# Performance work log

Measured on AMD Instinct MI355X. Metric: run time of the kernel, lower is better.

Reference implementation:

```python
import jax, jax.numpy as jnp
import numpy as np

N_NODES = 100000
N_EDGES = 3200000
N_GRAPHS = 64
NEG_SLOPE = 0.2


def mish(x):
    return x * jnp.tanh(jax.nn.softplus(x))


def gat_layer(x, src, dst, W, b, a_src, a_dst, heads, out_ch, n_nodes):
    # h: [N, H, C]
    h = (x @ W).reshape(n_nodes, heads, out_ch)
    alpha_s = jnp.sum(h * a_src[None], axis=-1)  # [N, H]
    alpha_d = jnp.sum(h * a_dst[None], axis=-1)  # [N, H]
    e = jax.nn.leaky_relu(alpha_s[src] + alpha_d[dst], NEG_SLOPE)  # [E, H]
    # scatter-softmax over incoming edges of each destination node
    emax = jax.ops.segment_max(e, dst, num_segments=n_nodes)  # [N, H]
    ee = jnp.exp(e - emax[dst])
    den = jax.ops.segment_sum(ee, dst, num_segments=n_nodes)
    alpha = ee / (den[dst] + 1e-16)  # [E, H]
    msg = h[src] * alpha[..., None]  # [E, H, C]
    out = jax.ops.segment_sum(msg, dst, num_segments=n_nodes)
    return out.reshape(n_nodes, heads * out_ch) + b


def setup_inputs() -> dict:
    key = jax.random.key(0)
    ks = jax.random.split(key, 10)
    x = jax.random.normal(ks[0], (N_NODES, 128), dtype=jnp.float32)
    edge_index = jax.random.randint(ks[1], (2, N_EDGES), 0, N_NODES, dtype=jnp.int64)
    batch = jnp.sort(jax.random.randint(ks[2], (N_NODES,), 0, N_GRAPHS, dtype=jnp.int64))
    s1 = 1.0 / np.sqrt(128.0)
    s2 = 1.0 / np.sqrt(16.0)
    return {
        "x": x,
        "edge_index": edge_index,
        "batch": batch,
        "W1": jax.random.normal(ks[3], (128, 16), dtype=jnp.float32) * s1,
        "b1": jnp.zeros((16,), dtype=jnp.float32),
        "a_src1": jax.random.normal(ks[4], (4, 4), dtype=jnp.float32) * 0.5,
        "a_dst1": jax.random.normal(ks[5], (4, 4), dtype=jnp.float32) * 0.5,
        "W2": jax.random.normal(ks[6], (16, 32), dtype=jnp.float32) * s2,
        "b2": jnp.zeros((32,), dtype=jnp.float32),
        "a_src2": jax.random.normal(ks[7], (1, 32), dtype=jnp.float32) * 0.5,
        "a_dst2": jax.random.normal(ks[8], (1, 32), dtype=jnp.float32) * 0.5,
    }


def reference(x, edge_index, batch, W1, b1, a_src1, a_dst1, W2, b2, a_src2, a_dst2):
    n = x.shape[0]
    # PyG GATConv default add_self_loops=True
    loop = jnp.arange(n, dtype=edge_index.dtype)
    src = jnp.concatenate([edge_index[0], loop])
    dst = jnp.concatenate([edge_index[1], loop])
    h = mish(gat_layer(x, src, dst, W1, b1, a_src1, a_dst1, heads=4, out_ch=4, n_nodes=n))
    h = mish(gat_layer(h, src, dst, W2, b2, a_src2, a_dst2, heads=1, out_ch=32, n_nodes=n))
    # global_mean_pool
    sums = jax.ops.segment_sum(h, batch, num_segments=N_GRAPHS)
    cnts = jax.ops.segment_sum(jnp.ones((n,), h.dtype), batch, num_segments=N_GRAPHS)
    return sums / jnp.maximum(cnts, 1.0)[:, None]
```

## Files before the change

kernel.cpp:

```cpp
#include <hip/hip_runtime.h>
#include <hip/hip_fp16.h>
#include <math.h>

#define NEG_SLOPE 0.2f
#define SB 256
#define NBMAX 1024

typedef _Float16 half2v __attribute__((ext_vector_type(2)));

__device__ __forceinline__ float mishf(float x) {
    if (x > 15.f) return x;
    float ex = __expf(x);
    float y = 1.f + ex;
    float y2 = y * y;
    return x * (y2 - 1.f) / (y2 + 1.f);
}

__device__ __forceinline__ float lw(float e) {
    return __expf(fmaxf(e, NEG_SLOPE * e));
}

__device__ __forceinline__ float hdot2(half2v a, half2v b) {
#if __has_builtin(__builtin_amdgcn_fdot2)
    return __builtin_amdgcn_fdot2(a, b, 0.f, false);
#else
    return (float)a.x * (float)b.x + (float)a.y * (float)b.y;
#endif
}

__global__ void gemm1_kernel(const float* __restrict__ x, const float* __restrict__ W1,
                             const float* __restrict__ a_dst,
                             _Float16* __restrict__ hpre1h, float* __restrict__ addst,
                             int* __restrict__ bucket_total, float* __restrict__ pool,
                             float* __restrict__ cnt, int NB, int NG, int N) {
    __shared__ float Wl[128 * 16];
    __shared__ float xs[16 * 132];
    int tid = threadIdx.x;
    if (blockIdx.x == 0) {
        for (int i = tid; i < NB; i += 256) bucket_total[i] = 0;
        for (int i = tid; i < NG * 32; i += 256) pool[i] = 0.f;
        for (int i = tid; i < NG; i += 256) cnt[i] = 0.f;
    }
    for (int i = tid; i < 2048; i += 256) Wl[i] = W1[i];
    int nodebase = blockIdx.x * 16;
    const float4* x4 = (const float4*)(x + (size_t)nodebase * 128);
    for (int i = tid; i < 512; i += 256) {
        float4 v = x4[i];
        int e = i * 4;
        int nl = e >> 7, k = e & 127;
        float* dp = &xs[nl * 132 + k];
        dp[0] = v.x; dp[1] = v.y; dp[2] = v.z; dp[3] = v.w;
    }
    __syncthreads();
    int nl = tid >> 4, ch = tid & 15;
    const float* xr = &xs[nl * 132];
    float acc = 0.f;
    #pragma unroll 8
    for (int k = 0; k < 128; k++) acc += xr[k] * Wl[k * 16 + ch];
    int node = nodebase + nl;
    if (node < N) {
        hpre1h[node * 16 + ch] = (_Float16)acc;
        float pd = acc * a_dst[ch];
        pd += __shfl_xor(pd, 1); pd += __shfl_xor(pd, 2);
        if ((ch & 3) == 0) addst[node * 4 + (ch >> 2)] = pd;
    }
}

__global__ __launch_bounds__(1024) void histB_kernel(
        const int* __restrict__ dst, int E, int Etot, int CH, int NB,
        int* __restrict__ hist, int* __restrict__ bucket_total) {
    __shared__ int cnt[NBMAX];
    int tid = threadIdx.x, blk = blockIdx.x;
    for (int b = tid; b < NB; b += 1024) cnt[b] = 0;
    __syncthreads();
    int iend = min((blk + 1) * CH, Etot);
    for (int i = blk * CH + tid; i < iend; i += 1024) {
        int d = (i < E) ? dst[i] : (i - E);
        atomicAdd(&cnt[d >> 7], 1);
    }
    __syncthreads();
    for (int b = tid; b < NB; b += 1024) {
        int c = cnt[b];
        hist[b * SB + blk] = c;
        if (c) atomicAdd(&bucket_total[b], c);
    }
}

__global__ __launch_bounds__(1024) void setup_kernel(
        const int* __restrict__ bucket_total, int NB,
        int* __restrict__ bucket_base, int* __restrict__ cursor,
        const float* __restrict__ W2, const float* __restrict__ as2,
        const float* __restrict__ ad2, float* __restrict__ vs, float* __restrict__ vd) {
    __shared__ int s[1024];
    int t = threadIdx.x;
    int own = (t < NB) ? bucket_total[t] : 0;
    s[t] = own;
    __syncthreads();
    for (int off = 1; off < 1024; off <<= 1) {
        int v = (t >= off) ? s[t - off] : 0;
        __syncthreads();
        s[t] += v;
        __syncthreads();
    }
    if (t < NB) {
        int ex = s[t] - own;
        bucket_base[t] = ex;
        cursor[t] = ex;
    }
    if (t < 16) {
        float ps = 0.f, pd = 0.f;
        #pragma unroll
        for (int c = 0; c < 32; c++) {
            float w = W2[t * 32 + c];
            ps += w * as2[c];
            pd += w * ad2[c];
        }
        vs[t] = ps; vd[t] = pd;
    }
}

__global__ __launch_bounds__(1024) void scatE2_kernel(
        const int* __restrict__ src, const int* __restrict__ dst,
        int E, int Etot, int CH, int NB,
        const int* __restrict__ hist, int* __restrict__ cursor,
        int* __restrict__ pairs) {
    __shared__ int lcnt[NBMAX];
    __shared__ int lbase[NBMAX];
    int tid = threadIdx.x, blk = blockIdx.x;
    for (int b = tid; b < NB; b += 1024) {
        lcnt[b] = 0;
        int h = hist[b * SB + blk];
        lbase[b] = h ? atomicAdd(&cursor[b], h) : 0;
    }
    __syncthreads();
    int iend = min((blk + 1) * CH, Etot);
    for (int i = blk * CH + tid; i < iend; i += 1024) {
        int s, d;
        if (i < E) { s = src[i]; d = dst[i]; } else { s = d = i - E; }
        int b = d >> 7, dl = d & 127;
        int r = atomicAdd(&lcnt[b], 1);
        pairs[lbase[b] + r] = s | (dl << 17);
    }
}

__global__ __launch_bounds__(1024) void localcsr_kernel(
        const int* __restrict__ pairs, const int* __restrict__ bucket_base,
        const int* __restrict__ bucket_total, int NB, int N,
        int* __restrict__ ssorted, int* __restrict__ row_start) {
    __shared__ int deg[128];
    __shared__ int s[128];
    __shared__ int cur[128];
    int tid = threadIdx.x, b = blockIdx.x;
    int nb0 = b << 7;
    int cnt_nodes = min(128, N - nb0);
    int start = bucket_base[b];
    int end = start + bucket_total[b];
    if (tid < 128) deg[tid] = 0;
    __syncthreads();
    for (int j = start + tid; j < end; j += 1024)
        atomicAdd(&deg[(pairs[j] >> 17) & 127], 1);
    __syncthreads();
    if (tid < 128) s[tid] = deg[tid];
    __syncthreads();
    for (int o = 1; o < 128; o <<= 1) {
        int v = 0;
        if (tid < 128 && tid >= o) v = s[tid - o];
        __syncthreads();
        if (tid < 128) s[tid] += v;
        __syncthreads();
    }
    if (tid < 128) {
        int ex = start + s[tid] - deg[tid];
        cur[tid] = ex;
        if (tid < cnt_nodes) row_start[nb0 + tid] = ex;
    }
    if (b == NB - 1 && tid == 0) row_start[N] = end;
    __syncthreads();
    for (int j = start + tid; j < end; j += 1024) {
        int p = pairs[j];
        int pos = atomicAdd(&cur[(p >> 17) & 127], 1);
        ssorted[pos] = p & 0x1FFFF;
    }
}

__global__ void agg1_kernel(const int* __restrict__ row_start, const int* __restrict__ ssorted,
                            const float* __restrict__ a_src1, const float* __restrict__ addst,
                            const _Float16* __restrict__ hpre1h,
                            const float* __restrict__ b1,
                            const float* __restrict__ vs, const float* __restrict__ vd,
                            _Float16* __restrict__ hpost1h,
                            float* __restrict__ as2n, float* __restrict__ ad2n, int N) {
    int wave = threadIdx.x >> 6;
    int lane = threadIdx.x & 63;
    int node = blockIdx.x * 4 + wave;
    if (node >= N) return;
    int start = row_start[node], end = row_start[node + 1];
    int er = lane >> 3, hc = lane & 7, head = hc >> 1;
    int c0 = hc * 2;
    half2v wsh;
    wsh.x = (_Float16)a_src1[c0];
    wsh.y = (_Float16)a_src1[c0 + 1];
    float adh = addst[node * 4 + head];
    const _Float16* hb = hpre1h + c0;
    float den = 0.f, a0 = 0.f, a1 = 0.f;
    int last = end - 1;
    int jb = start;
    for (; jb + 16 <= end; jb += 16) {
        int j0 = jb + er, j1 = j0 + 8;
        int s0 = __builtin_nontemporal_load(ssorted + j0);
        int s1 = __builtin_nontemporal_load(ssorted + j1);
        half2v h0 = *(const half2v*)(hb + s0 * 16);
        half2v h1 = *(const half2v*)(hb + s1 * 16);
        float p0 = hdot2(h0, wsh);
        float p1 = hdot2(h1, wsh);
        float w0 = lw(p0 + __shfl_xor(p0, 1) + adh);
        float w1 = lw(p1 + __shfl_xor(p1, 1) + adh);
        den += w0 + w1;
        a0 += (float)h0.x * w0 + (float)h1.x * w1;
        a1 += (float)h0.y * w0 + (float)h1.y * w1;
    }
    if (jb < end) {
        int j0 = jb + er, j1 = j0 + 8;
        int k0 = (j0 <= last) ? j0 : last;
        int k1 = (j1 <= last) ? j1 : last;
        int s0 = __builtin_nontemporal_load(ssorted + k0);
        int s1 = __builtin_nontemporal_load(ssorted + k1);
        half2v h0 = *(const half2v*)(hb + s0 * 16);
        half2v h1 = *(const half2v*)(hb + s1 * 16);
        float p0 = hdot2(h0, wsh);
        float p1 = hdot2(h1, wsh);
        float e0 = p0 + __shfl_xor(p0, 1) + adh;
        float e1 = p1 + __shfl_xor(p1, 1) + adh;
        float w0 = (j0 <= last) ? lw(e0) : 0.f;
        float w1 = (j1 <= last) ? lw(e1) : 0.f;
        den += w0 + w1;
        a0 += (float)h0.x * w0 + (float)h1.x * w1;
        a1 += (float)h0.y * w0 + (float)h1.y * w1;
    }
    a0 += __shfl_xor(a0, 8);  a1 += __shfl_xor(a1, 8);  den += __shfl_xor(den, 8);
    a0 += __shfl_xor(a0, 16); a1 += __shfl_xor(a1, 16); den += __shfl_xor(den, 16);
    a0 += __shfl_xor(a0, 32); a1 += __shfl_xor(a1, 32); den += __shfl_xor(den, 32);
    if (er == 0) {
        float inv = 1.f / (den + 1e-16f);
        float o0 = mishf(a0 * inv + b1[c0]);
        float o1 = mishf(a1 * inv + b1[c0 + 1]);
        half2v oh;
        oh.x = (_Float16)o0; oh.y = (_Float16)o1;
        *(half2v*)(hpost1h + node * 16 + c0) = oh;
        float ps = o0 * vs[c0] + o1 * vs[c0 + 1];
        float pd = o0 * vd[c0] + o1 * vd[c0 + 1];
        ps += __shfl_xor(ps, 1); pd += __shfl_xor(pd, 1);
        ps += __shfl_xor(ps, 2); pd += __shfl_xor(pd, 2);
        ps += __shfl_xor(ps, 4); pd += __shfl_xor(pd, 4);
        if (hc == 0) { as2n[node] = ps; ad2n[node] = pd; }
    }
}

__global__ void agg2_kernel(const int* __restrict__ row_start, const int* __restrict__ ssorted,
                            const float* __restrict__ as2n, const float* __restrict__ ad2n,
                            const _Float16* __restrict__ hpost1h,
                            float* __restrict__ agg16, float* __restrict__ denv, int N) {
    int wave = threadIdx.x >> 6;
    int lane = threadIdx.x & 63;
    int node = blockIdx.x * 4 + wave;
    if (node >= N) return;
    int start = row_start[node], end = row_start[node + 1];
    int er = lane >> 3, hc = lane & 7;
    int c0 = hc * 2;
    float adh = ad2n[node];
    const _Float16* hb = hpost1h + c0;
    float den = 0.f, a0 = 0.f, a1 = 0.f;
    int last = end - 1;
    int jb = start;
    for (; jb + 16 <= end; jb += 16) {
        int j0 = jb + er, j1 = j0 + 8;
        int s0 = __builtin_nontemporal_load(ssorted + j0);
        int s1 = __builtin_nontemporal_load(ssorted + j1);
        float e0 = as2n[s0] + adh;
        float e1 = as2n[s1] + adh;
        half2v h0 = *(const half2v*)(hb + s0 * 16);
        half2v h1 = *(const half2v*)(hb + s1 * 16);
        float w0 = lw(e0);
        float w1 = lw(e1);
        den += w0 + w1;
        a0 += (float)h0.x * w0 + (float)h1.x * w1;
        a1 += (float)h0.y * w0 + (float)h1.y * w1;
    }
    if (jb < end) {
        int j0 = jb + er, j1 = j0 + 8;
        int k0 = (j0 <= last) ? j0 : last;
        int k1 = (j1 <= last) ? j1 : last;
        int s0 = __builtin_nontemporal_load(ssorted + k0);
        int s1 = __builtin_nontemporal_load(ssorted + k1);
        float e0 = as2n[s0] + adh;
        float e1 = as2n[s1] + adh;
        half2v h0 = *(const half2v*)(hb + s0 * 16);
        half2v h1 = *(const half2v*)(hb + s1 * 16);
        float w0 = (j0 <= last) ? lw(e0) : 0.f;
        float w1 = (j1 <= last) ? lw(e1) : 0.f;
        den += w0 + w1;
        a0 += (float)h0.x * w0 + (float)h1.x * w1;
        a1 += (float)h0.y * w0 + (float)h1.y * w1;
    }
    a0 += __shfl_xor(a0, 8);  a1 += __shfl_xor(a1, 8);  den += __shfl_xor(den, 8);
    a0 += __shfl_xor(a0, 16); a1 += __shfl_xor(a1, 16); den += __shfl_xor(den, 16);
    a0 += __shfl_xor(a0, 32); a1 += __shfl_xor(a1, 32); den += __shfl_xor(den, 32);
    if (er == 0) {
        float2 o; o.x = a0; o.y = a1;
        *(float2*)(agg16 + node * 16 + c0) = o;
        if (hc == 0) denv[node] = den;
    }
}

__global__ void post2_kernel(const float* __restrict__ agg16, const float* __restrict__ denv,
                             const float* __restrict__ W2, const float* __restrict__ b2,
                             float* __restrict__ hpost2, int N) {
    __shared__ float Wl[16 * 32];
    __shared__ float hs[8 * 20];
    __shared__ float dsh[8];
    int tid = threadIdx.x;
    for (int i = tid; i < 512; i += 256) Wl[i] = W2[i];
    int nodebase = blockIdx.x * 8;
    const float4* h4 = (const float4*)(agg16 + (size_t)nodebase * 16);
    if (tid < 32) {
        float4 v = h4[tid];
        int e = tid * 4;
        int nl = e >> 4, k = e & 15;
        float* dp = &hs[nl * 20 + k];
        dp[0] = v.x; dp[1] = v.y; dp[2] = v.z; dp[3] = v.w;
    }
    if (tid < 8) {
        int n = nodebase + tid;
        dsh[tid] = denv[(n < N) ? n : (N - 1)];
    }
    __syncthreads();
    int nl = tid >> 5, ch = tid & 31;
    const float* hr = &hs[nl * 20];
    float acc = 0.f;
    #pragma unroll
    for (int k = 0; k < 16; k++) acc += hr[k] * Wl[k * 32 + ch];
    int node = nodebase + nl;
    if (node < N) {
        float val = acc / (dsh[nl] + 1e-16f) + b2[ch];
        hpost2[(size_t)node * 32 + ch] = mishf(val);
    }
}

__global__ void pool_kernel(const float* __restrict__ hpost2, const int* __restrict__ batch,
                            int N, float* __restrict__ pool, float* __restrict__ cnt) {
    int tid = threadIdx.x;
    int r = tid >> 5, ch = tid & 31;
    int base = blockIdx.x * 512;
    int cur = -1;
    float sum = 0.f, c = 0.f;
    for (int it = 0; it < 64; it++) {
        int n = base + it * 8 + r;
        if (n >= N) break;
        int g = batch[n];
        if (g != cur) {
            if (cur >= 0) {
                atomicAdd(&pool[cur * 32 + ch], sum);
                if (ch == 0) atomicAdd(&cnt[cur], c);
            }
            cur = g; sum = 0.f; c = 0.f;
        }
        sum += hpost2[(size_t)n * 32 + ch];
        c += 1.f;
    }
    if (cur >= 0) {
        atomicAdd(&pool[cur * 32 + ch], sum);
        if (ch == 0) atomicAdd(&cnt[cur], c);
    }
}

__global__ void fin_kernel(const float* __restrict__ pool, const float* __restrict__ cnt,
                           float* __restrict__ out, int NG) {
    int i = blockIdx.x * blockDim.x + threadIdx.x;
    if (i >= NG * 32) return;
    out[i] = pool[i] / fmaxf(cnt[i >> 5], 1.0f);
}

extern "C" void kernel_launch(void* const* d_in, const int* in_sizes, int n_in,
                              void* d_out, int out_size, void* d_ws, size_t ws_size,
                              hipStream_t stream) {
    const float* x   = (const float*)d_in[0];
    const int* eidx  = (const int*)d_in[1];
    const int* batch = (const int*)d_in[2];
    const float* W1  = (const float*)d_in[3];
    const float* b1  = (const float*)d_in[4];
    const float* as1 = (const float*)d_in[5];
    const float* ad1 = (const float*)d_in[6];
    const float* W2  = (const float*)d_in[7];
    const float* b2  = (const float*)d_in[8];
    const float* as2 = (const float*)d_in[9];
    const float* ad2 = (const float*)d_in[10];
    float* out = (float*)d_out;

    int N = in_sizes[0] / 128;
    int E = in_sizes[1] / 2;
    int Etot = E + N;
    int NG = out_size / 32;
    const int* esrc = eidx;
    const int* edst = eidx + E;

    int NB = (N + 127) >> 7;
    int CH = (Etot + SB - 1) / SB;
    int T  = NB * SB;

    char* p = (char*)d_ws;
    auto alloc = [&](size_t nbytes) {
        p = (char*)(((uintptr_t)p + 15) & ~(uintptr_t)15);
        void* r = (void*)p; p += nbytes; return r;
    };
    int* hist         = (int*)alloc((size_t)T * 4);
    int* pairs        = (int*)alloc((size_t)Etot * 4);
    int* ssorted      = (int*)alloc((size_t)Etot * 4);
    int* row_start    = (int*)alloc((size_t)(N + 1) * 4);
    int* bucket_total = (int*)alloc((size_t)NB * 4);
    int* bucket_base  = (int*)alloc((size_t)NB * 4);
    int* cursor       = (int*)alloc((size_t)NB * 4);
    _Float16* hpre1h  = (_Float16*)alloc((size_t)N * 16 * 2);
    _Float16* hpost1h = (_Float16*)alloc((size_t)N * 16 * 2);
    float* addst1  = (float*)alloc((size_t)N * 4 * 4);
    float* as2n    = (float*)alloc((size_t)N * 4);
    float* ad2n    = (float*)alloc((size_t)N * 4);
    float* agg16   = (float*)alloc((size_t)N * 16 * 4);
    float* denv    = (float*)alloc((size_t)N * 4);
    float* hpost2  = (float*)alloc((size_t)N * 32 * 4);
    float* vs      = (float*)alloc(16 * 4);
    float* vd      = (float*)alloc(16 * 4);
    float* pool    = (float*)alloc((size_t)NG * 32 * 4);
    float* cnt     = (float*)alloc((size_t)NG * 4);

    gemm1_kernel<<<(N + 15) / 16, 256, 0, stream>>>(x, W1, ad1, hpre1h, addst1,
                                                    bucket_total, pool, cnt, NB, NG, N);
    histB_kernel<<<SB, 1024, 0, stream>>>(edst, E, Etot, CH, NB, hist, bucket_total);
    setup_kernel<<<1, 1024, 0, stream>>>(bucket_total, NB, bucket_base, cursor,
                                         W2, as2, ad2, vs, vd);
    scatE2_kernel<<<SB, 1024, 0, stream>>>(esrc, edst, E, Etot, CH, NB, hist, cursor, pairs);
    localcsr_kernel<<<NB, 1024, 0, stream>>>(pairs, bucket_base, bucket_total, NB, N,
                                             ssorted, row_start);
    agg1_kernel<<<(N + 3) / 4, 256, 0, stream>>>(row_start, ssorted, as1, addst1, hpre1h,
                                                 b1, vs, vd, hpost1h, as2n, ad2n, N);
    agg2_kernel<<<(N + 3) / 4, 256, 0, stream>>>(row_start, ssorted, as2n, ad2n, hpost1h,
                                                 agg16, denv, N);
    post2_kernel<<<(N + 7) / 8, 256, 0, stream>>>(agg16, denv, W2, b2, hpost2, N);
    pool_kernel<<<(N + 511) / 512, 256, 0, stream>>>(hpost2, batch, N, pool, cnt);
    fin_kernel<<<(NG * 32 + 255) / 256, 256, 0, stream>>>(pool, cnt, out, NG);
}
```

Before: 377.5 us.

## Fuse CSR build with layer-1 aggregation and post2 with pooling

The local CSR construction kernel now goes straight on to aggregate layer 1 for its 128-node bucket. Each of its 16 waves handles 8 nodes, reading the edge slice just written to ssorted, which is likely still in cache. The post-GEMM/mish of layer 2 is folded into the pooling kernel, so the N×32 hpost2 buffer is no longer written and re-read. Fewer launches and less memory traffic are traded for less parallelism in agg1 (782 blocks of 1024 threads) and serialized node processing per wave.

Measured after the change: 372.0 us. Within noise of the previous version (-1.4%).

```diff
diff --git a/kernel.cpp b/kernel.cpp
--- a/kernel.cpp
+++ b/kernel.cpp
@@ -143,21 +143,26 @@
     }
 }
 
-__global__ __launch_bounds__(1024) void localcsr_kernel(
+__global__ __launch_bounds__(1024) void csragg1_kernel(
         const int* __restrict__ pairs, const int* __restrict__ bucket_base,
         const int* __restrict__ bucket_total, int NB, int N,
-        int* __restrict__ ssorted, int* __restrict__ row_start) {
+        int* __restrict__ ssorted, int* __restrict__ row_start,
+        const float* __restrict__ a_src1, const float* __restrict__ addst,
+        const _Float16* __restrict__ hpre1h, const float* __restrict__ b1,
+        const float* __restrict__ vs, const float* __restrict__ vd,
+        _Float16* __restrict__ hpost1h,
+        float* __restrict__ as2n, float* __restrict__ ad2n) {
     __shared__ int deg[128];
     __shared__ int s[128];
     __shared__ int cur[128];
     int tid = threadIdx.x, b = blockIdx.x;
     int nb0 = b << 7;
     int cnt_nodes = min(128, N - nb0);
-    int start = bucket_base[b];
-    int end = start + bucket_total[b];
+    int bstart = bucket_base[b];
+    int bend = bstart + bucket_total[b];
     if (tid < 128) deg[tid] = 0;
     __syncthreads();
-    for (int j = start + tid; j < end; j += 1024)
+    for (int j = bstart + tid; j < bend; j += 1024)
         atomicAdd(&deg[(pairs[j] >> 17) & 127], 1);
     __syncthreads();
     if (tid < 128) s[tid] = deg[tid];
@@ -170,89 +175,86 @@
         __syncthreads();
     }
     if (tid < 128) {
-        int ex = start + s[tid] - deg[tid];
+        int ex = bstart + s[tid] - deg[tid];
         cur[tid] = ex;
         if (tid < cnt_nodes) row_start[nb0 + tid] = ex;
     }
-    if (b == NB - 1 && tid == 0) row_start[N] = end;
-    __syncthreads();
-    for (int j = start + tid; j < end; j += 1024) {
+    if (b == NB - 1 && tid == 0) row_start[N] = bend;
+    __syncthreads();
+    for (int j = bstart + tid; j < bend; j += 1024) {
         int p = pairs[j];
         int pos = atomicAdd(&cur[(p >> 17) & 127], 1);
         ssorted[pos] = p & 0x1FFFF;
     }
-}
-
-__global__ void agg1_kernel(const int* __restrict__ row_start, const int* __restrict__ ssorted,
-                            const float* __restrict__ a_src1, const float* __restrict__ addst,
-                            const _Float16* __restrict__ hpre1h,
-                            const float* __restrict__ b1,
-                            const float* __restrict__ vs, const float* __restrict__ vd,
-                            _Float16* __restrict__ hpost1h,
-                            float* __restrict__ as2n, float* __restrict__ ad2n, int N) {
-    int wave = threadIdx.x >> 6;
-    int lane = threadIdx.x & 63;
-    int node = blockIdx.x * 4 + wave;
-    if (node >= N) return;
-    int start = row_start[node], end = row_start[node + 1];
+    __syncthreads();
+
+    int wave = tid >> 6;
+    int lane = tid & 63;
     int er = lane >> 3, hc = lane & 7, head = hc >> 1;
     int c0 = hc * 2;
     half2v wsh;
     wsh.x = (_Float16)a_src1[c0];
     wsh.y = (_Float16)a_src1[c0 + 1];
-    float adh = addst[node * 4 + head];
     const _Float16* hb = hpre1h + c0;
-    float den = 0.f, a0 = 0.f, a1 = 0.f;
-    int last = end - 1;
-    int jb = start;
-    for (; jb + 16 <= end; jb += 16) {
-        int j0 = jb + er, j1 = j0 + 8;
-        int s0 = __builtin_nontemporal_load(ssorted + j0);
-        int s1 = __builtin_nontemporal_load(ssorted + j1);
-        half2v h0 = *(const half2v*)(hb + s0 * 16);
-        half2v h1 = *(const half2v*)(hb + s1 * 16);
-        float p0 = hdot2(h0, wsh);
-        float p1 = hdot2(h1, wsh);
-        float w0 = lw(p0 + __shfl_xor(p0, 1) + adh);
-        float w1 = lw(p1 + __shfl_xor(p1, 1) + adh);
-        den += w0 + w1;
-        a0 += (float)h0.x * w0 + (float)h1.x * w1;
-        a1 += (float)h0.y * w0 + (float)h1.y * w1;
-    }
-    if (jb < end) {
-        int j0 = jb + er, j1 = j0 + 8;
-        int k0 = (j0 <= last) ? j0 : last;
-        int k1 = (j1 <= last) ? j1 : last;
-        int s0 = __builtin_nontemporal_load(ssorted + k0);
-        int s1 = __builtin_nontemporal_load(ssorted + k1);
-        half2v h0 = *(const half2v*)(hb + s0 * 16);
-        half2v h1 = *(const half2v*)(hb + s1 * 16);
-        float p0 = hdot2(h0, wsh);
-        float p1 = hdot2(h1, wsh);
-        float e0 = p0 + __shfl_xor(p0, 1) + adh;
-        float e1 = p1 + __shfl_xor(p1, 1) + adh;
-        float w0 = (j0 <= last) ? lw(e0) : 0.f;
-        float w1 = (j1 <= last) ? lw(e1) : 0.f;
-        den += w0 + w1;
-        a0 += (float)h0.x * w0 + (float)h1.x * w1;
-        a1 += (float)h0.y * w0 + (float)h1.y * w1;
-    }
-    a0 += __shfl_xor(a0, 8);  a1 += __shfl_xor(a1, 8);  den += __shfl_xor(den, 8);
-    a0 += __shfl_xor(a0, 16); a1 += __shfl_xor(a1, 16); den += __shfl_xor(den, 16);
-    a0 += __shfl_xor(a0, 32); a1 += __shfl_xor(a1, 32); den += __shfl_xor(den, 32);
-    if (er == 0) {
-        float inv = 1.f / (den + 1e-16f);
-        float o0 = mishf(a0 * inv + b1[c0]);
-        float o1 = mishf(a1 * inv + b1[c0 + 1]);
-        half2v oh;
-        oh.x = (_Float16)o0; oh.y = (_Float16)o1;
-        *(half2v*)(hpost1h + node * 16 + c0) = oh;
-        float ps = o0 * vs[c0] + o1 * vs[c0 + 1];
-        float pd = o0 * vd[c0] + o1 * vd[c0 + 1];
-        ps += __shfl_xor(ps, 1); pd += __shfl_xor(pd, 1);
-        ps += __shfl_xor(ps, 2); pd += __shfl_xor(pd, 2);
-        ps += __shfl_xor(ps, 4); pd += __shfl_xor(pd, 4);
-        if (hc == 0) { as2n[node] = ps; ad2n[node] = pd; }
+    for (int r = 0; r < 8; r++) {
+        int ln = (wave << 3) + r;
+        if (ln >= cnt_nodes) break;
+        int node = nb0 + ln;
+        int end = cur[ln];
+        int start = end - deg[ln];
+        float adh = addst[node * 4 + head];
+        float den = 0.f, a0 = 0.f, a1 = 0.f;
+        int last = end - 1;
+        int jb = start;
+        for (; jb + 16 <= end; jb += 16) {
+            int j0 = jb + er, j1 = j0 + 8;
+            int s0 = ssorted[j0];
+            int s1 = ssorted[j1];
+            half2v h0 = *(const half2v*)(hb + s0 * 16);
+            half2v h1 = *(const half2v*)(hb + s1 * 16);
+            float p0 = hdot2(h0, wsh);
+            float p1 = hdot2(h1, wsh);
+            float w0 = lw(p0 + __shfl_xor(p0, 1) + adh);
+            float w1 = lw(p1 + __shfl_xor(p1, 1) + adh);
+            den += w0 + w1;
+            a0 += (float)h0.x * w0 + (float)h1.x * w1;
+            a1 += (float)h0.y * w0 + (float)h1.y * w1;
+        }
+        if (jb < end) {
+            int j0 = jb + er, j1 = j0 + 8;
+            int k0 = (j0 <= last) ? j0 : last;
+            int k1 = (j1 <= last) ? j1 : last;
+            int s0 = ssorted[k0];
+            int s1 = ssorted[k1];
+            half2v h0 = *(const half2v*)(hb + s0 * 16);
+            half2v h1 = *(const half2v*)(hb + s1 * 16);
+            float p0 = hdot2(h0, wsh);
+            float p1 = hdot2(h1, wsh);
+            float e0 = p0 + __shfl_xor(p0, 1) + adh;
+            float e1 = p1 + __shfl_xor(p1, 1) + adh;
+            float w0 = (j0 <= last) ? lw(e0) : 0.f;
+            float w1 = (j1 <= last) ? lw(e1) : 0.f;
+            den += w0 + w1;
+            a0 += (float)h0.x * w0 + (float)h1.x * w1;
+            a1 += (float)h0.y * w0 + (float)h1.y * w1;
+        }
+        a0 += __shfl_xor(a0, 8);  a1 += __shfl_xor(a1, 8);  den += __shfl_xor(den, 8);
+        a0 += __shfl_xor(a0, 16); a1 += __shfl_xor(a1, 16); den += __shfl_xor(den, 16);
+        a0 += __shfl_xor(a0, 32); a1 += __shfl_xor(a1, 32); den += __shfl_xor(den, 32);
+        if (er == 0) {
+            float inv = 1.f / (den + 1e-16f);
+            float o0 = mishf(a0 * inv + b1[c0]);
+            float o1 = mishf(a1 * inv + b1[c0 + 1]);
+            half2v oh;
+            oh.x = (_Float16)o0; oh.y = (_Float16)o1;
+            *(half2v*)(hpost1h + node * 16 + c0) = oh;
+            float ps = o0 * vs[c0] + o1 * vs[c0 + 1];
+            float pd = o0 * vd[c0] + o1 * vd[c0 + 1];
+            ps += __shfl_xor(ps, 1); pd += __shfl_xor(pd, 1);
+            ps += __shfl_xor(ps, 2); pd += __shfl_xor(pd, 2);
+            ps += __shfl_xor(ps, 4); pd += __shfl_xor(pd, 4);
+            if (hc == 0) { as2n[node] = ps; ad2n[node] = pd; }
+        }
     }
 }
 
@@ -312,44 +314,16 @@
     }
 }
 
-__global__ void post2_kernel(const float* __restrict__ agg16, const float* __restrict__ denv,
-                             const float* __restrict__ W2, const float* __restrict__ b2,
-                             float* __restrict__ hpost2, int N) {
+__global__ void post2pool_kernel(const float* __restrict__ agg16, const float* __restrict__ denv,
+                                 const float* __restrict__ W2, const float* __restrict__ b2,
+                                 const int* __restrict__ batch,
+                                 float* __restrict__ pool, float* __restrict__ cnt, int N) {
     __shared__ float Wl[16 * 32];
-    __shared__ float hs[8 * 20];
-    __shared__ float dsh[8];
     int tid = threadIdx.x;
     for (int i = tid; i < 512; i += 256) Wl[i] = W2[i];
-    int nodebase = blockIdx.x * 8;
-    const float4* h4 = (const float4*)(agg16 + (size_t)nodebase * 16);
-    if (tid < 32) {
-        float4 v = h4[tid];
-        int e = tid * 4;
-        int nl = e >> 4, k = e & 15;
-        float* dp = &hs[nl * 20 + k];
-        dp[0] = v.x; dp[1] = v.y; dp[2] = v.z; dp[3] = v.w;
-    }
-    if (tid < 8) {
-        int n = nodebase + tid;
-        dsh[tid] = denv[(n < N) ? n : (N - 1)];
-    }
-    __syncthreads();
-    int nl = tid >> 5, ch = tid & 31;
-    const float* hr = &hs[nl * 20];
-    float acc = 0.f;
-    #pragma unroll
-    for (int k = 0; k < 16; k++) acc += hr[k] * Wl[k * 32 + ch];
-    int node = nodebase + nl;
-    if (node < N) {
-        float val = acc / (dsh[nl] + 1e-16f) + b2[ch];
-        hpost2[(size_t)node * 32 + ch] = mishf(val);
-    }
-}
-
-__global__ void pool_kernel(const float* __restrict__ hpost2, const int* __restrict__ batch,
-                            int N, float* __restrict__ pool, float* __restrict__ cnt) {
-    int tid = threadIdx.x;
+    __syncthreads();
     int r = tid >> 5, ch = tid & 31;
+    float bc = b2[ch];
     int base = blockIdx.x * 512;
     int cur = -1;
     float sum = 0.f, c = 0.f;
@@ -364,7 +338,12 @@
             }
             cur = g; sum = 0.f; c = 0.f;
         }
-        sum += hpost2[(size_t)n * 32 + ch];
+        const float* ar = agg16 + (size_t)n * 16;
+        float acc = 0.f;
+        #pragma unroll
+        for (int k = 0; k < 16; k++) acc += ar[k] * Wl[k * 32 + ch];
+        float val = mishf(acc / (denv[n] + 1e-16f) + bc);
+        sum += val;
         c += 1.f;
     }
     if (cur >= 0) {
@@ -426,7 +405,6 @@
     float* ad2n    = (float*)alloc((size_t)N * 4);
     float* agg16   = (float*)alloc((size_t)N * 16 * 4);
     float* denv    = (float*)alloc((size_t)N * 4);
-    float* hpost2  = (float*)alloc((size_t)N * 32 * 4);
     float* vs      = (float*)alloc(16 * 4);
     float* vd      = (float*)alloc(16 * 4);
     float* pool    = (float*)alloc((size_t)NG * 32 * 4);
@@ -438,13 +416,12 @@
     setup_kernel<<<1, 1024, 0, stream>>>(bucket_total, NB, bucket_base, cursor,
                                          W2, as2, ad2, vs, vd);
     scatE2_kernel<<<SB, 1024, 0, stream>>>(esrc, edst, E, Etot, CH, NB, hist, cursor, pairs);
-    localcsr_kernel<<<NB, 1024, 0, stream>>>(pairs, bucket_base, bucket_total, NB, N,
-                                             ssorted, row_start);
-    agg1_kernel<<<(N + 3) / 4, 256, 0, stream>>>(row_start, ssorted, as1, addst1, hpre1h,
-                                                 b1, vs, vd, hpost1h, as2n, ad2n, N);
+    csragg1_kernel<<<NB, 1024, 0, stream>>>(pairs, bucket_base, bucket_total, NB, N,
+                                            ssorted, row_start, as1, addst1, hpre1h,
+                                            b1, vs, vd, hpost1h, as2n, ad2n);
     agg2_kernel<<<(N + 3) / 4, 256, 0, stream>>>(row_start, ssorted, as2n, ad2n, hpost1h,
                                                  agg16, denv, N);
-    post2_kernel<<<(N + 7) / 8, 256, 0, stream>>>(agg16, denv, W2, b2, hpost2, N);
-    pool_kernel<<<(N + 511) / 512, 256, 0, stream>>>(hpost2, batch, N, pool, cnt);
+    post2pool_kernel<<<(N + 511) / 512, 256, 0, stream>>>(agg16, denv, W2, b2, batch,
+                                                          pool, cnt, N);
     fin_kernel<<<(NG * 32 + 255) / 256, 256, 0, stream>>>(pool, cnt, out, NG);
 }
```
